# Performance work log

Measured on AMD Instinct MI355X. Metric: run time of the kernel, lower is better.

The kernel has to match this reference:

```python
import jax, jax.numpy as jnp
import numpy as np

VOCAB = 256     # input_dim (one_hot depth)
EMBED = 256     # output_dim
BATCH = 32
SEQ = 8192


def setup_inputs() -> dict:
    key = jax.random.key(0)
    k_ids, k_w = jax.random.split(key)
    inputs = jax.random.randint(k_ids, (BATCH, SEQ), 0, VOCAB, dtype=jnp.int32)
    # SmallNormal initializer: small-stddev normal weights
    kernel = 0.02 * jax.random.normal(k_w, (VOCAB, EMBED), dtype=jnp.float32)
    return {"inputs": inputs, "kernel": kernel}


def reference(inputs, kernel):
    # Original: tf.matmul(tf.one_hot(inputs, depth=VOCAB, dtype=f32), kernel)
    # one_hot @ kernel is mathematically an embedding gather: out[b,s,:] = kernel[inputs[b,s],:]
    return jnp.take(kernel, inputs, axis=0)  # [BATCH, SEQ, EMBED]
```

## Files before the change

### kernel.cpp

```cpp
#include <hip/hip_runtime.h>
#include <hip/hip_bf16.h>


#define EMBED 256
#define CHUNKS_PER_ROW (EMBED / 4)
#define ROWS_PER_WAVE 64
#define WAVES_PER_BLOCK 4

__global__ __launch_bounds__(256) void embedding_gather_kernel(
    const int* __restrict__ indices,
    const uint4* __restrict__ table,
    uint4* __restrict__ out,
    int tokens)
{
    const int lane    = threadIdx.x & 63;
    const int wave_id = blockIdx.x * WAVES_PER_BLOCK + (threadIdx.x >> 6);
    const int row_base = wave_id * ROWS_PER_WAVE;
    if (row_base >= tokens) return;

    int my_idx = 0;
    if (row_base + lane < tokens) my_idx = indices[row_base + lane];

    const int rows = (tokens - row_base < ROWS_PER_WAVE) ? (tokens - row_base)
                                                         : ROWS_PER_WAVE;

    #pragma unroll 4
    for (int i = 0; i < rows; ++i) {
        const int idx = __builtin_amdgcn_readlane(my_idx, i);
        const uint4 v = table[(size_t)idx * CHUNKS_PER_ROW + lane];
        out[((size_t)row_base + i) * CHUNKS_PER_ROW + lane] = v;
    }
}

extern "C" void kernel_launch(void* const* d_in, const int* in_sizes, int n_in,
                              void* d_out, int out_size, void* d_ws, size_t ws_size,
                              hipStream_t stream) {
    const int*   indices = (const int*)d_in[0];
    const uint4* table   = (const uint4*)d_in[1];
    uint4*       out     = (uint4*)d_out;

    const int tokens = in_sizes[0];
    const int waves  = (tokens + ROWS_PER_WAVE - 1) / ROWS_PER_WAVE;
    const int blocks = (waves + WAVES_PER_BLOCK - 1) / WAVES_PER_BLOCK;

    embedding_gather_kernel<<<blocks, 256, 0, stream>>>(indices, table, out, tokens);
}
```

Measured before the change: 254.5 us.

## Double-buffer gathered rows in registers and halve rows per wave

Each wave now handles 32 rows instead of 64 and loads table rows in groups of eight into two register buffers. The next group's loads are issued before the current group is stored, keeping more memory requests in flight. Partial waves fall back to a simple loop. This costs higher register use, and the index load per row is used less efficiently.

```diff
diff --git a/kernel.cpp b/kernel.cpp
--- a/kernel.cpp
+++ b/kernel.cpp
@@ -1,34 +1,70 @@
 #include <hip/hip_runtime.h>
-#include <hip/hip_bf16.h>
 
 
 #define EMBED 256
 #define CHUNKS_PER_ROW (EMBED / 4)
-#define ROWS_PER_WAVE 64
+#define ROWS_PER_WAVE 32
 #define WAVES_PER_BLOCK 4
+#define G 8
+
+typedef unsigned int u32x4 __attribute__((ext_vector_type(4)));
 
 __global__ __launch_bounds__(256) void embedding_gather_kernel(
     const int* __restrict__ indices,
-    const uint4* __restrict__ table,
-    uint4* __restrict__ out,
+    const u32x4* __restrict__ table,
+    u32x4* __restrict__ out,
     int tokens)
 {
     const int lane    = threadIdx.x & 63;
     const int wave_id = blockIdx.x * WAVES_PER_BLOCK + (threadIdx.x >> 6);
-    const int row_base = wave_id * ROWS_PER_WAVE;
+    const long row_base = (long)wave_id * ROWS_PER_WAVE;
     if (row_base >= tokens) return;
 
     int my_idx = 0;
     if (row_base + lane < tokens) my_idx = indices[row_base + lane];
 
-    const int rows = (tokens - row_base < ROWS_PER_WAVE) ? (tokens - row_base)
-                                                         : ROWS_PER_WAVE;
+    const u32x4* __restrict__ tb  = table + lane;
+    u32x4* __restrict__       dst = out + (size_t)row_base * CHUNKS_PER_ROW + lane;
 
-    #pragma unroll 4
-    for (int i = 0; i < rows; ++i) {
-        const int idx = __builtin_amdgcn_readlane(my_idx, i);
-        const uint4 v = table[(size_t)idx * CHUNKS_PER_ROW + lane];
-        out[((size_t)row_base + i) * CHUNKS_PER_ROW + lane] = v;
+    const long rem  = tokens - row_base;
+    const int  rows = rem < ROWS_PER_WAVE ? (int)rem : ROWS_PER_WAVE;
+
+    if (rows == ROWS_PER_WAVE) {
+        u32x4 bufA[G], bufB[G];
+
+        #pragma unroll
+        for (int g = 0; g < G; ++g) {
+            const int idx = __builtin_amdgcn_readlane(my_idx, g);
+            bufA[g] = tb[(size_t)idx * CHUNKS_PER_ROW];
+        }
+
+        #pragma unroll
+        for (int i = 0; i < ROWS_PER_WAVE; i += 2 * G) {
+            #pragma unroll
+            for (int g = 0; g < G; ++g) {
+                const int idx = __builtin_amdgcn_readlane(my_idx, i + G + g);
+                bufB[g] = tb[(size_t)idx * CHUNKS_PER_ROW];
+            }
+            #pragma unroll
+            for (int g = 0; g < G; ++g)
+                dst[(size_t)(i + g) * CHUNKS_PER_ROW] = bufA[g];
+
+            if (i + 2 * G < ROWS_PER_WAVE) {
+                #pragma unroll
+                for (int g = 0; g < G; ++g) {
+                    const int idx = __builtin_amdgcn_readlane(my_idx, i + 2 * G + g);
+                    bufA[g] = tb[(size_t)idx * CHUNKS_PER_ROW];
+                }
+            }
+            #pragma unroll
+            for (int g = 0; g < G; ++g)
+                dst[(size_t)(i + G + g) * CHUNKS_PER_ROW] = bufB[g];
+        }
+    } else {
+        for (int i = 0; i < rows; ++i) {
+            const int idx = __builtin_amdgcn_readlane(my_idx, i);
+            dst[(size_t)i * CHUNKS_PER_ROW] = tb[(size_t)idx * CHUNKS_PER_ROW];
+        }
     }
 }
 
@@ -36,8 +72,8 @@
                               void* d_out, int out_size, void* d_ws, size_t ws_size,
                               hipStream_t stream) {
     const int*   indices = (const int*)d_in[0];
-    const uint4* table   = (const uint4*)d_in[1];
-    uint4*       out     = (uint4*)d_out;
+    const u32x4* table   = (const u32x4*)d_in[1];
+    u32x4*       out     = (u32x4*)d_out;
 
     const int tokens = in_sizes[0];
     const int waves  = (tokens + ROWS_PER_WAVE - 1) / ROWS_PER_WAVE;
```

After: 251.3 us. No clear change (-1.3%).
